# Kernel tuning notes

Hardware: AMD Instinct MI355X
Metric: run time of the kernel (lower is better)

The kernel has to match this reference:

```python
import jax, jax.numpy as jnp
import numpy as np

L, B, S, M, D, H, DK, FF = 4, 2, 512, 512, 1024, 16, 64, 4096


def setup_inputs() -> dict:
    key = jax.random.key(0)
    ks = jax.random.split(key, 16)
    std = 0.02
    inp = {
        'x': jax.random.normal(ks[0], (B, S, D), jnp.float32),
        'memory': jax.random.normal(ks[1], (L, B, M, D), jnp.float32),
        'Wq': jax.random.normal(ks[2], (L, D, D), jnp.float32) * std,
        'Wk': jax.random.normal(ks[3], (L, D, D), jnp.float32) * std,
        'Wv': jax.random.normal(ks[4], (L, D, D), jnp.float32) * std,
        'Wr': jax.random.normal(ks[5], (L, D, D), jnp.float32) * std,
        'Wo': jax.random.normal(ks[6], (L, D, D), jnp.float32) * std,
        'r_w_bias': jax.random.normal(ks[7], (L, H, DK), jnp.float32) * std,
        'r_r_bias': jax.random.normal(ks[8], (L, H, DK), jnp.float32) * std,
        'ln1_g': jnp.ones((L, D), jnp.float32),
        'ln1_b': jnp.zeros((L, D), jnp.float32),
        'ln2_g': jnp.ones((L, D), jnp.float32),
        'ln2_b': jnp.zeros((L, D), jnp.float32),
        'W1': jax.random.normal(ks[9], (L, D, FF), jnp.float32) * std,
        'b1': jnp.zeros((L, FF), jnp.float32),
        'W2': jax.random.normal(ks[10], (L, FF, D), jnp.float32) * std,
        'b2': jnp.zeros((L, D), jnp.float32),
    }
    return inp


def _pos_encodings(length, hidden):
    # sinusoidal encodings over [length-1 .. 0], sin/cos concat -> [length, hidden]
    pos = jnp.arange(length - 1, -1, -1, dtype=jnp.float32)
    freqs = jnp.arange(0, hidden, 2, dtype=jnp.float32)
    inv_freq = 1.0 / (10000.0 ** (freqs / hidden))
    ang = pos[:, None] * inv_freq[None, :]  # [T, D/2]
    return jnp.concatenate([jnp.sin(ang), jnp.cos(ang)], axis=-1)  # [T, D]


def _rel_shift(x):
    # x: [B, H, T1, T2] -> Transformer-XL relative shift
    b, h, t1, t2 = x.shape
    x = jnp.pad(x, ((0, 0), (0, 0), (0, 0), (1, 0)))
    x = x.reshape(b, h, t2 + 1, t1)[:, :, 1:]
    return x.reshape(b, h, t1, t2)


def _layernorm(x, g, b, eps=1e-5):
    mu = jnp.mean(x, axis=-1, keepdims=True)
    var = jnp.var(x, axis=-1, keepdims=True)
    return (x - mu) * jax.lax.rsqrt(var + eps) * g + b


def reference(x, memory, Wq, Wk, Wv, Wr, Wo, r_w_bias, r_r_bias,
              ln1_g, ln1_b, ln2_g, ln2_b, W1, b1, W2, b2):
    T = S + M
    pos = _pos_encodings(T, D)  # [T, D]
    # future mask with zero block for memory columns: [1,1,S,T]
    fut = jnp.triu(jnp.ones((S, S), jnp.float32), k=1) * (-1e6)
    mask = jnp.concatenate([jnp.zeros((S, M), jnp.float32), fut], axis=1)[None, None]
    scale = DK ** (-0.5)

    h = x
    for l in range(L):
        kv_in = jnp.concatenate([memory[l], h], axis=1)  # [B, T, D]
        q = jnp.einsum('bsd,dhk->bhsk', h, Wq[l].reshape(D, H, DK)) * scale
        k = jnp.einsum('btd,dhk->bhtk', kv_in, Wk[l].reshape(D, H, DK))
        v = jnp.einsum('btd,dhk->bhtk', kv_in, Wv[l].reshape(D, H, DK))
        r = jnp.einsum('td,dhk->htk', pos, Wr[l].reshape(D, H, DK))

        content = jnp.einsum('bhsk,bhtk->bhst', q + r_w_bias[l][None, :, None, :], k)
        rel = jnp.einsum('bhsk,htk->bhst', q + r_r_bias[l][None, :, None, :], r)
        logits = content + _rel_shift(rel) + mask  # [B,H,S,T]
        w = jax.nn.softmax(logits, axis=-1)
        attn = jnp.einsum('bhst,bhtk->bshk', w, v).reshape(B, S, D)
        attn = attn @ Wo[l]  # merge linear
        h = _layernorm(h + attn, ln1_g[l], ln1_b[l])

        ff = jax.nn.relu(h @ W1[l] + b1[l]) @ W2[l] + b2[l]
        h = _layernorm(h + ff, ln2_g[l], ln2_b[l])
    return h
```

## Files before the change

kernel.cpp:

```cpp
#include <hip/hip_runtime.h>
#include <math.h>

#define CB  2
#define CS  512
#define CM  512
#define CD  1024
#define CH  16
#define CDK 64
#define CFF 4096
#define CL  4
#define CT  1024

using short8 = __attribute__((ext_vector_type(8))) short;
using f32x4  = __attribute__((ext_vector_type(4))) float;

__device__ __forceinline__ ushort f2bf(float x) {
    union { float f; unsigned int u; } c; c.f = x;
    unsigned int u = c.u + 0x7FFFu + ((c.u >> 16) & 1u);
    return (ushort)(u >> 16);
}
__device__ __forceinline__ float bf2f(ushort h) {
    union { unsigned int u; float f; } c; c.u = ((unsigned int)h) << 16;
    return c.f;
}

#define GLD16(gsrc, ldst) \
    __builtin_amdgcn_global_load_lds((const __attribute__((address_space(1))) void*)(gsrc), \
                                     (__attribute__((address_space(3))) void*)(ldst), 16, 0, 0)

__global__ void pos_kernel(ushort* __restrict__ pos) {
    int idx = blockIdx.x * blockDim.x + threadIdx.x;
    if (idx >= CT * (CD / 2)) return;
    int i = idx % (CD / 2);
    int t = idx / (CD / 2);
    float p = (float)(CT - 1 - t);
    float inv = __expf(-(float)i * (9.210340371976184f / 512.0f));
    float ang = p * inv;
    pos[(size_t)t * CD + i]          = f2bf(sinf(ang));
    pos[(size_t)t * CD + i + CD / 2] = f2bf(cosf(ang));
}

__global__ void cvt_bf16_kernel(const float* __restrict__ in, ushort* __restrict__ out, int n8) {
    int i = blockIdx.x * blockDim.x + threadIdx.x;
    if (i >= n8) return;
    float4 a = ((const float4*)in)[i * 2];
    float4 c = ((const float4*)in)[i * 2 + 1];
    union { ushort us[8]; uint4 q; } pk;
    pk.us[0] = f2bf(a.x); pk.us[1] = f2bf(a.y); pk.us[2] = f2bf(a.z); pk.us[3] = f2bf(a.w);
    pk.us[4] = f2bf(c.x); pk.us[5] = f2bf(c.y); pk.us[6] = f2bf(c.z); pk.us[7] = f2bf(c.w);
    ((uint4*)out)[i] = pk.q;
}

__global__ __launch_bounds__(256)
void transpose_w5(const float* __restrict__ Wq, const float* __restrict__ Wk,
                  const float* __restrict__ Wv, const float* __restrict__ Wr,
                  const float* __restrict__ Wo,
                  ushort* __restrict__ wqkvT, ushort* __restrict__ wrT,
                  ushort* __restrict__ woT) {
    const size_t WD = (size_t)CD * CD;
    const int wi = blockIdx.z / CL, l = blockIdx.z % CL;
    const float* in;
    ushort* o;
    float sc = 1.0f;
    switch (wi) {
        case 0: in = Wq + l * WD; o = wqkvT + (size_t)l * 3 * WD; sc = 0.125f; break;
        case 1: in = Wk + l * WD; o = wqkvT + (size_t)l * 3 * WD + WD; break;
        case 2: in = Wv + l * WD; o = wqkvT + (size_t)l * 3 * WD + 2 * WD; break;
        case 3: in = Wr + l * WD; o = wrT + (size_t)l * WD; break;
        default: in = Wo + l * WD; o = woT + (size_t)l * WD; break;
    }
    __shared__ __align__(16) float t[64][68];
    const int n0 = blockIdx.x * 64, k0 = blockIdx.y * 64;
    const int tid = threadIdx.x;
    #pragma unroll
    for (int rep = 0; rep < 4; ++rep) {
        int lin = rep * 256 + tid;
        int r = lin >> 4, c4 = lin & 15;
        float4 v = *(const float4*)&in[(size_t)(k0 + r) * CD + n0 + c4 * 4];
        *(float4*)&t[r][c4 * 4] = v;
    }
    __syncthreads();
    #pragma unroll
    for (int rep = 0; rep < 2; ++rep) {
        int lin = rep * 256 + tid;
        int n = lin >> 3, kc = lin & 7;
        union { ushort us[8]; uint4 q; } pk;
        #pragma unroll
        for (int j = 0; j < 8; ++j) pk.us[j] = f2bf(t[kc * 8 + j][n] * sc);
        *(uint4*)&o[(size_t)(n0 + n) * CD + k0 + kc * 8] = pk.q;
    }
}

__global__ __launch_bounds__(256)
void transpose_cvt(const float* __restrict__ inb, ushort* __restrict__ outb,
                   int Kd, int Nc, size_t inz, size_t outz) {
    const float* in = inb + (size_t)blockIdx.z * inz;
    ushort* o = outb + (size_t)blockIdx.z * outz;
    __shared__ __align__(16) float t[64][68];
    const int n0 = blockIdx.x * 64, k0 = blockIdx.y * 64;
    const int tid = threadIdx.x;
    #pragma unroll
    for (int rep = 0; rep < 4; ++rep) {
        int lin = rep * 256 + tid;
        int r = lin >> 4, c4 = lin & 15;
        float4 v = *(const float4*)&in[(size_t)(k0 + r) * Nc + n0 + c4 * 4];
        *(float4*)&t[r][c4 * 4] = v;
    }
    __syncthreads();
    #pragma unroll
    for (int rep = 0; rep < 2; ++rep) {
        int lin = rep * 256 + tid;
        int n = lin >> 3, kc = lin & 7;
        union { ushort us[8]; uint4 q; } pk;
        #pragma unroll
        for (int j = 0; j < 8; ++j) pk.us[j] = f2bf(t[kc * 8 + j][n]);
        *(uint4*)&o[(size_t)(n0 + n) * Kd + k0 + kc * 8] = pk.q;
    }
}

template<int BM, int BN>
__global__ __launch_bounds__(256)
void gemm_bf16(const ushort* __restrict__ A, const ushort* __restrict__ Bt,
               float* __restrict__ Cf, ushort* __restrict__ Cbf,
               int Nc, int Kd, int lda, int cw, int ch,
               size_t az, size_t bz, size_t cz,
               const float* __restrict__ bias, float scale, int relu)
{
    constexpr int FM = BM / 32, FN = BN / 32;
    __shared__ __align__(16) ushort As[2][BM * 64];
    __shared__ __align__(16) ushort Bs[2][BN * 64];
    const int tid  = threadIdx.x;
    const int lane = tid & 63, w = tid >> 6;
    const int wr = w >> 1, wc = w & 1;
    const int lo4 = lane & 15, g = lane >> 4;
    const int id  = blockIdx.y * gridDim.x + blockIdx.x;
    const int e = id & 7, q = id >> 3;
    const int ncx = gridDim.x / cw;
    const int col0 = ((e % ncx) * cw + q % cw) * BN;
    const int row0 = ((e / ncx) * ch + q / cw) * BM;
    const int zz = blockIdx.z;
    const ushort* Ab = A  + (size_t)row0 * lda + (size_t)zz * az;
    const ushort* Bb = Bt + (size_t)col0 * lda + (size_t)zz * bz;
    f32x4 acc[FM][FN];
    #pragma unroll
    for (int m = 0; m < FM; ++m)
        #pragma unroll
        for (int n = 0; n < FN; ++n) acc[m][n] = (f32x4){0.f, 0.f, 0.f, 0.f};

#define GSTAGE(buf, kk) do {                                                          \
        _Pragma("unroll")                                                             \
        for (int c = 0; c < BM / 32; ++c) {                                           \
            const int linw = (c * 4 + w) * 64;                                        \
            const int lin  = linw + lane;                                             \
            GLD16(Ab + (size_t)(lin >> 3) * lda + (kk) + ((lin ^ (lin >> 3)) & 7) * 8, \
                  &As[buf][linw * 8]);                                                \
        }                                                                             \
        _Pragma("unroll")                                                             \
        for (int c = 0; c < BN / 32; ++c) {                                           \
            const int linw = (c * 4 + w) * 64;                                        \
            const int lin  = linw + lane;                                             \
            GLD16(Bb + (size_t)(lin >> 3) * lda + (kk) + ((lin ^ (lin >> 3)) & 7) * 8, \
                  &Bs[buf][linw * 8]);                                                \
        }                                                                             \
    } while (0)

    GSTAGE(0, 0);
    __syncthreads();
    int cur = 0;
    for (int k0 = 0; k0 < Kd; k0 += 64) {
        if (k0 + 64 < Kd) GSTAGE(cur ^ 1, k0 + 64);
        #pragma unroll
        for (int h2 = 0; h2 < 2; ++h2) {
            short8 af[FM], bfr[FN];
            #pragma unroll
            for (int m = 0; m < FM; ++m) {
                const int ar = wr * (BM / 2) + m * 16 + lo4;
                af[m] = *(const short8*)&As[cur][ar * 64 + ((((h2 << 2) + g) ^ (ar & 7)) << 3)];
            }
            #pragma unroll
            for (int n = 0; n < FN; ++n) {
                const int br = wc * (BN / 2) + n * 16 + lo4;
                bfr[n] = *(const short8*)&Bs[cur][br * 64 + ((((h2 << 2) + g) ^ (br & 7)) << 3)];
            }
            __builtin_amdgcn_s_setprio(1);
            #pragma unroll
            for (int m = 0; m < FM; ++m)
                #pragma unroll
                for (int n = 0; n < FN; ++n)
                    acc[m][n] = __builtin_amdgcn_mfma_f32_16x16x32_bf16(af[m], bfr[n], acc[m][n], 0, 0, 0);
            __builtin_amdgcn_s_setprio(0);
        }
        __syncthreads();
        cur ^= 1;
    }
#undef GSTAGE

    float*  Cw  = Cf  ? Cf  + (size_t)zz * cz : nullptr;
    ushort* Cbw = Cbf ? Cbf + (size_t)zz * cz : nullptr;
    const int colbase = col0 + wc * (BN / 2) + lo4;
    const int rowbase = row0 + wr * (BM / 2) + (g << 2);
    #pragma unroll
    for (int n = 0; n < FN; ++n) {
        const int col = colbase + n * 16;
        const float bv = bias ? bias[col] : 0.f;
        #pragma unroll
        for (int m = 0; m < FM; ++m) {
            #pragma unroll
            for (int r = 0; r < 4; ++r) {
                const int row = rowbase + m * 16 + r;
                float v = acc[m][n][r] * scale + bv;
                if (relu) v = fmaxf(v, 0.f);
                if (Cw)  Cw[(size_t)row * Nc + col] = v;
                if (Cbw) Cbw[(size_t)row * Nc + col] = f2bf(v);
            }
        }
    }
}

__global__ __launch_bounds__(256, 4)
void attn_kernel(const ushort* __restrict__ hproj, const ushort* __restrict__ kvmem,
                 const ushort* __restrict__ rbm,
                 const float* __restrict__ rwb, const float* __restrict__ rrb,
                 float* __restrict__ pw)
{
    const int id  = blockIdx.y * 32 + blockIdx.x;
    const int swz = (id & 7) * 64 + (id >> 3);
    const int zt = (swz & 31) >> 1, js = swz & 1;
    const int hh = swz >> 5, bb = blockIdx.z;
    const int q0 = zt * 32;
    __shared__ __align__(16) ushort Ks[64 * 64];
    __shared__ __align__(16) ushort Rs[96 * 64];
    __shared__ __align__(16) ushort Vt[80][72];
    __shared__ __align__(16) ushort Pl[4][16][40];
    __shared__ float mB[2][16], lB[2][16];
    const int tid = threadIdx.x;
    const int lane = tid & 63, w = tid >> 6;
    const int iw = w & 1, jh = w >> 1;
    const int g = lane >> 4, lo4 = lane & 15;

    for (int idx = tid; idx < 16 * 36; idx += 256)
        *(uint*)&Vt[64 + idx / 36][(idx % 36) * 2] = 0x3F803F80u;

    short8 aqw[2], aqr[2];
    {
        const ushort* qrow = hproj + ((size_t)(bb * CS + q0 + iw * 16 + lo4)) * 3072 + hh * CDK;
        const float* bw = rwb + hh * CDK;
        const float* br = rrb + hh * CDK;
        #pragma unroll
        for (int c = 0; c < 2; ++c) {
            const int kb = c * 32 + g * 8;
            uint4 qv = *(const uint4*)&qrow[kb];
            const ushort* qe = (const ushort*)&qv;
            #pragma unroll
            for (int e = 0; e < 8; ++e) {
                float qf = bf2f(qe[e]);
                aqw[c][e] = (short)f2bf(qf + bw[kb + e]);
                aqr[c][e] = (short)f2bf(qf + br[kb + e]);
            }
        }
    }

    const ushort* kvmB = kvmem + (size_t)bb * CM * 2048;
    const ushort* hpjB = hproj + (size_t)bb * CS * 3072;
    const ushort* rb2  = rbm + hh * CDK;
    const int jp = tid & 31, c8v = tid >> 5;

    float mr[4] = {-1e29f, -1e29f, -1e29f, -1e29f};
    f32x4 oacc[5];
    #pragma unroll
    for (int n = 0; n < 5; ++n) oacc[n] = (f32x4){0.f, 0.f, 0.f, 0.f};

    const int nt   = (q0 + 31 + CM) / 64 + 1;
    const int half = nt >> 1;
    const int t0 = js ? half : 0;
    const int t1 = js ? nt : half;

    for (int tt = t0; tt < t1; ++tt) {
        const int j0 = tt * 64;
        const int bnd = j0 + 480 - q0;
        const int isMem = (j0 < CM);
        const ushort* kb2 = isMem ? (kvmB + hh * CDK) : (hpjB + 1024 + hh * CDK);
        const ushort* vb2 = isMem ? (kvmB + 1024 + hh * CDK) : (hpjB + 2048 + hh * CDK);
        const int rstr = isMem ? 2048 : 3072;
        const int jloc = isMem ? j0 : (j0 - CM);
        __syncthreads();
        #pragma unroll
        for (int c = 0; c < 2; ++c) {
            const int linw = (c * 4 + w) * 64;
            const int lin  = linw + lane;
            const int row = lin >> 3, kc = lin & 7;
            GLD16(kb2 + (size_t)(jloc + row) * rstr + ((kc ^ (row & 7)) * 8),
                  Ks + linw * 8);
        }
        #pragma unroll
        for (int rep = 0; rep < 3; ++rep) {
            const int linw = (rep * 4 + w) * 64;
            const int lin  = linw + lane;
            const int row = lin >> 3, kc = lin & 7;
            int trel = bnd + row;
            trel = trel < 0 ? 0 : (trel > CT - 1 ? CT - 1 : trel);
            GLD16(rb2 + (size_t)trel * CD + ((kc ^ (row & 7)) * 8),
                  Rs + linw * 8);
        }
        {
            uint4 v0 = *(const uint4*)(vb2 + (size_t)(jloc + 2 * jp) * rstr + c8v * 8);
            uint4 v1 = *(const uint4*)(vb2 + (size_t)(jloc + 2 * jp + 1) * rstr + c8v * 8);
            const ushort* p0 = (const ushort*)&v0;
            const ushort* p1 = (const ushort*)&v1;
            #pragma unroll
            for (int e = 0; e < 8; ++e)
                *(uint*)&Vt[c8v * 8 + e][2 * jp] = (uint)p0[e] | ((uint)p1[e] << 16);
        }
        __syncthreads();

        f32x4 sa[2];
        sa[0] = (f32x4){0.f, 0.f, 0.f, 0.f};
        sa[1] = (f32x4){0.f, 0.f, 0.f, 0.f};
        f32x4 ra[3];
        #pragma unroll
        for (int mm = 0; mm < 3; ++mm) ra[mm] = (f32x4){0.f, 0.f, 0.f, 0.f};
        const int wb16 = jh * 32 - iw * 16 + 16;
        __builtin_amdgcn_s_setprio(1);
        #pragma unroll
        for (int c = 0; c < 2; ++c) {
            #pragma unroll
            for (int m16 = 0; m16 < 2; ++m16) {
                const int krow = jh * 32 + m16 * 16 + lo4;
                short8 bk = *(const short8*)&Ks[krow * 64 + ((((c << 2) + g) ^ (krow & 7)) << 3)];
                sa[m16] = __builtin_amdgcn_mfma_f32_16x16x32_bf16(aqw[c], bk, sa[m16], 0, 0, 0);
            }
            #pragma unroll
            for (int mm = 0; mm < 3; ++mm) {
                const int rrow = wb16 + mm * 16 + lo4;
                short8 brr = *(const short8*)&Rs[rrow * 64 + ((((c << 2) + g) ^ (rrow & 7)) << 3)];
                ra[mm] = __builtin_amdgcn_mfma_f32_16x16x32_bf16(aqr[c], brr, ra[mm], 0, 0, 0);
            }
        }
        __builtin_amdgcn_s_setprio(0);

        #pragma unroll
        for (int r = 0; r < 4; ++r) {
            const int il = 4 * g + r;
            const int dlo = lo4 + 15 - il;
            const int srcl = (lane & 48) | (dlo & 15);
            const int hi = dlo >> 4;
            float va = __shfl(ra[0][r], srcl);
            float vb = __shfl(ra[1][r], srcl);
            float vc = __shfl(ra[2][r], srcl);
            const float rel0 = hi ? vb : va;
            const float rel1 = hi ? vc : vb;
            const int ig = q0 + iw * 16 + il;
            const int jbase = j0 + jh * 32 + lo4;
            float s0 = (jbase      <= ig + CM) ? (sa[0][r] + rel0) : -1e30f;
            float s1 = (jbase + 16 <= ig + CM) ? (sa[1][r] + rel1) : -1e30f;
            float tm = fmaxf(s0, s1);
            #pragma unroll
            for (int off = 1; off < 16; off <<= 1) tm = fmaxf(tm, __shfl_xor(tm, off));
            const float mn = fmaxf(mr[r], tm);
            const float scl = __expf(mr[r] - mn);
            mr[r] = mn;
            Pl[w][il][lo4]      = f2bf(__expf(s0 - mn));
            Pl[w][il][16 + lo4] = f2bf(__expf(s1 - mn));
            #pragma unroll
            for (int n = 0; n < 5; ++n) oacc[n][r] *= scl;
        }

        __builtin_amdgcn_s_setprio(1);
        {
            short8 pa = *(const short8*)&Pl[w][lo4][g * 8];
            #pragma unroll
            for (int n = 0; n < 4; ++n) {
                short8 vb = *(const short8*)&Vt[n * 16 + lo4][jh * 32 + g * 8];
                oacc[n] = __builtin_amdgcn_mfma_f32_16x16x32_bf16(pa, vb, oacc[n], 0, 0, 0);
            }
            short8 vo = *(const short8*)&Vt[64 + lo4][jh * 32 + g * 8];
            oacc[4] = __builtin_amdgcn_mfma_f32_16x16x32_bf16(pa, vo, oacc[4], 0, 0, 0);
        }
        __builtin_amdgcn_s_setprio(0);
    }

    __syncthreads();
    float* oTmp = (float*)&Rs[0];
    if (jh == 1) {
        #pragma unroll
        for (int r = 0; r < 4; ++r) {
            const int il = 4 * g + r;
            #pragma unroll
            for (int n = 0; n < 4; ++n)
                oTmp[((iw * 16 + il) << 6) + n * 16 + lo4] = oacc[n][r];
            if (lo4 == 0) { mB[iw][il] = mr[r]; lB[iw][il] = oacc[4][r]; }
        }
    }
    __syncthreads();
    if (jh == 0) {
        float* pwp = pw + ((size_t)(((bb * CH + hh) * 16 + zt) * 2 + js)) * 2112;
        #pragma unroll
        for (int r = 0; r < 4; ++r) {
            const int il = 4 * g + r;
            const int row = iw * 16 + il;
            const float mBv = mB[iw][il], lBv = lB[iw][il];
            const float ms = fmaxf(mr[r], mBv);
            const float fA = __expf(mr[r] - ms);
            const float fB = __expf(mBv - ms);
            const float lt = oacc[4][r] * fA + lBv * fB;
            #pragma unroll
            for (int n = 0; n < 4; ++n)
                pwp[(row << 6) + n * 16 + lo4] =
                    oacc[n][r] * fA + oTmp[(row << 6) + n * 16 + lo4] * fB;
            if (lo4 == 0) { pwp[2048 + row] = ms; pwp[2048 + 32 + row] = lt; }
        }
    }
}

__global__ __launch_bounds__(256)
void attn_merge(const float* __restrict__ pw, ushort* __restrict__ outm) {
    const int zt = blockIdx.x, hh = blockIdx.y, bb = blockIdx.z;
    const int tid = threadIdx.x;
    const int row = tid >> 3, c8 = tid & 7;
    const float* pA = pw + ((size_t)(((bb * CH + hh) * 16 + zt) * 2 + 0)) * 2112;
    const float* pB = pA + 2112;
    const float mA = pA[2048 + row], lA = pA[2048 + 32 + row];
    const float mBv = pB[2048 + row], lBv = pB[2048 + 32 + row];
    const float ms = fmaxf(mA, mBv);
    const float fA = __expf(mA - ms);
    const float fB = __expf(mBv - ms);
    const float invl = 1.0f / (lA * fA + lBv * fB);
    float4 a0 = *(const float4*)&pA[(row << 6) + c8 * 8];
    float4 a1 = *(const float4*)&pA[(row << 6) + c8 * 8 + 4];
    float4 b0 = *(const float4*)&pB[(row << 6) + c8 * 8];
    float4 b1 = *(const float4*)&pB[(row << 6) + c8 * 8 + 4];
    union { ushort us[8]; uint4 q; } pk;
    pk.us[0] = f2bf((a0.x * fA + b0.x * fB) * invl);
    pk.us[1] = f2bf((a0.y * fA + b0.y * fB) * invl);
    pk.us[2] = f2bf((a0.z * fA + b0.z * fB) * invl);
    pk.us[3] = f2bf((a0.w * fA + b0.w * fB) * invl);
    pk.us[4] = f2bf((a1.x * fA + b1.x * fB) * invl);
    pk.us[5] = f2bf((a1.y * fA + b1.y * fB) * invl);
    pk.us[6] = f2bf((a1.z * fA + b1.z * fB) * invl);
    pk.us[7] = f2bf((a1.w * fA + b1.w * fB) * invl);
    *(uint4*)&outm[((size_t)(bb * CS + zt * 32 + row)) * CD + hh * CDK + c8 * 8] = pk.q;
}

__global__ __launch_bounds__(256)
void ln_kernel(const float* __restrict__ a, const float* __restrict__ p0,
               const float* __restrict__ p1, const float* __restrict__ bias,
               const float* __restrict__ g, const float* __restrict__ beta,
               float* __restrict__ out, ushort* __restrict__ outbf)
{
    const int row = blockIdx.x;
    const int tid = threadIdx.x;
    const size_t base = (size_t)row * CD;
    float4 xa = *(const float4*)&a[base + tid * 4];
    float4 x0v = *(const float4*)&p0[base + tid * 4];
    float4 x1v = *(const float4*)&p1[base + tid * 4];
    float4 bb = bias ? *(const float4*)&bias[tid * 4] : make_float4(0.f, 0.f, 0.f, 0.f);
    float x0 = xa.x + x0v.x + x1v.x + bb.x;
    float x1 = xa.y + x0v.y + x1v.y + bb.y;
    float x2 = xa.z + x0v.z + x1v.z + bb.z;
    float x3 = xa.w + x0v.w + x1v.w + bb.w;
    float sum = x0 + x1 + x2 + x3;
    float sq  = x0 * x0 + x1 * x1 + x2 * x2 + x3 * x3;
    #pragma unroll
    for (int off = 1; off < 64; off <<= 1) {
        sum += __shfl_xor(sum, off);
        sq  += __shfl_xor(sq, off);
    }
    __shared__ float ssum[4], ssq[4];
    const int wid = tid >> 6;
    if ((tid & 63) == 0) { ssum[wid] = sum; ssq[wid] = sq; }
    __syncthreads();
    sum = ssum[0] + ssum[1] + ssum[2] + ssum[3];
    sq  = ssq[0] + ssq[1] + ssq[2] + ssq[3];
    const float mean = sum * (1.0f / CD);
    const float var  = sq * (1.0f / CD) - mean * mean;
    const float rstd = rsqrtf(var + 1e-5f);
    float4 gv = *(const float4*)&g[tid * 4];
    float4 bv = *(const float4*)&beta[tid * 4];
    float4 r;
    r.x = (x0 - mean) * rstd * gv.x + bv.x;
    r.y = (x1 - mean) * rstd * gv.y + bv.y;
    r.z = (x2 - mean) * rstd * gv.z + bv.z;
    r.w = (x3 - mean) * rstd * gv.w + bv.w;
    *(float4*)&out[base + tid * 4] = r;
    if (outbf) {
        union { ushort us[4]; uint2 q; } pk;
        pk.us[0] = f2bf(r.x); pk.us[1] = f2bf(r.y); pk.us[2] = f2bf(r.z); pk.us[3] = f2bf(r.w);
        *(uint2*)&outbf[base + tid * 4] = pk.q;
    }
}

extern "C" void kernel_launch(void* const* d_in, const int* in_sizes, int n_in,
                              void* d_out, int out_size, void* d_ws, size_t ws_size,
                              hipStream_t stream) {
    const float* x    = (const float*)d_in[0];
    const float* memL = (const float*)d_in[1];
    const float* Wq   = (const float*)d_in[2];
    const float* Wk   = (const float*)d_in[3];
    const float* Wv   = (const float*)d_in[4];
    const float* Wr   = (const float*)d_in[5];
    const float* Wo   = (const float*)d_in[6];
    const float* rwb  = (const float*)d_in[7];
    const float* rrb  = (const float*)d_in[8];
    const float* ln1g = (const float*)d_in[9];
    const float* ln1b = (const float*)d_in[10];
    const float* ln2g = (const float*)d_in[11];
    const float* ln2b = (const float*)d_in[12];
    const float* W1   = (const float*)d_in[13];
    const float* b1   = (const float*)d_in[14];
    const float* W2   = (const float*)d_in[15];
    const float* b2   = (const float*)d_in[16];

    const size_t MEG = 1048576;
    float* h      = (float*)d_ws;
    float* p0     = h + MEG;
    float* p1     = p0 + MEG;
    float* pw     = p1 + MEG;
    ushort* hbf   = (ushort*)(pw + 1024 * 2112);
    ushort* membf = hbf + MEG;
    ushort* kvmem = membf + 4 * MEG;
    ushort* hproj = kvmem + 8 * MEG;
    ushort* attbf = hproj + 3 * MEG;
    ushort* ff1bf = attbf + MEG;
    ushort* posbf = ff1bf + 4 * MEG;
    ushort* r_all = posbf + MEG;
    ushort* wqkvT = r_all + 4 * MEG;
    ushort* wrT   = wqkvT + 12 * MEG;
    ushort* woT   = wrT + 4 * MEG;
    ushort* w1T   = woT + 4 * MEG;
    ushort* w2T   = w1T + 16 * MEG;

    const size_t WD = (size_t)CD * CD;

    pos_kernel<<<(CT * (CD / 2)) / 256, 256, 0, stream>>>(posbf);
    cvt_bf16_kernel<<<(CL * CB * CM * CD / 8) / 256, 256, 0, stream>>>(
        memL, membf, CL * CB * CM * CD / 8);
    cvt_bf16_kernel<<<(CB * CS * CD / 8) / 256, 256, 0, stream>>>(
        x, hbf, CB * CS * CD / 8);
    transpose_w5<<<dim3(16, 16, 5 * CL), 256, 0, stream>>>(Wq, Wk, Wv, Wr, Wo, wqkvT, wrT, woT);
    transpose_cvt<<<dim3(64, 16, CL), 256, 0, stream>>>(W1, w1T, CD, CFF, 4 * WD, 4 * WD);
    transpose_cvt<<<dim3(16, 64, CL), 256, 0, stream>>>(W2, w2T, CFF, CD, 4 * WD, 4 * WD);
    gemm_bf16<64, 64><<<dim3(16, 16, CL), 256, 0, stream>>>(
        posbf, wrT, nullptr, r_all, CD, CD, CD, 4, 8, 0, WD, (size_t)CT * CD,
        nullptr, 1.0f, 0);
    gemm_bf16<64, 128><<<dim3(16, 16, CL), 256, 0, stream>>>(
        membf, wqkvT + WD, nullptr, kvmem,
        2 * CD, CD, CD, 4, 8, MEG, 3 * WD, 2 * MEG, nullptr, 1.0f, 0);

    for (int l = 0; l < CL; ++l) {
        const float* hin = (l == 0) ? x : h;

        gemm_bf16<64, 128><<<dim3(24, 16), 256, 0, stream>>>(
            hbf, wqkvT + (size_t)l * 3 * WD, nullptr, hproj,
            3 * CD, CD, CD, 6, 8, 0, 0, 0, nullptr, 1.0f, 0);

        attn_kernel<<<dim3(2 * CS / 32, CH, CB), 256, 0, stream>>>(
            hproj, kvmem + (size_t)l * 2 * MEG, r_all + (size_t)l * CT * CD,
            rwb + (size_t)l * CH * CDK, rrb + (size_t)l * CH * CDK, pw);
        attn_merge<<<dim3(CS / 32, CH, CB), 256, 0, stream>>>(pw, attbf);

        gemm_bf16<64, 64><<<dim3(16, 16, 2), 256, 0, stream>>>(
            attbf, woT + (size_t)l * WD, p0, nullptr,
            CD, CD / 2, CD, 4, 8, CD / 2, CD / 2, MEG, nullptr, 1.0f, 0);
        ln_kernel<<<CB * CS, 256, 0, stream>>>(
            hin, p0, p1, nullptr, ln1g + (size_t)l * CD, ln1b + (size_t)l * CD, h, hbf);

        gemm_bf16<64, 128><<<dim3(32, 16), 256, 0, stream>>>(
            hbf, w1T + (size_t)l * 4 * WD, nullptr, ff1bf,
            CFF, CD, CD, 8, 8, 0, 0, 0, b1 + (size_t)l * CFF, 1.0f, 1);
        gemm_bf16<64, 64><<<dim3(16, 16, 2), 256, 0, stream>>>(
            ff1bf, w2T + (size_t)l * 4 * WD, p0, nullptr,
            CD, CFF / 2, CFF, 4, 8, CFF / 2, CFF / 2, MEG, nullptr, 1.0f, 0);
        ln_kernel<<<CB * CS, 256, 0, stream>>>(
            h, p0, p1, b2 + (size_t)l * CD, ln2g + (size_t)l * CD, ln2b + (size_t)l * CD,
            (l == CL - 1) ? (float*)d_out : h,
            (l == CL - 1) ? nullptr : hbf);
    }
}
```

Measured before the change: 597.6 us.

## Switch bf16 GEMM to a four-stage 32-wide K pipeline with explicit vmcnt waits

Replaces the double-buffered 64-wide K tile with a four-deep ring of 32-wide K tiles, using a new XOR swizzle for the narrower rows. Explicit s_waitcnt vmcnt and raw barriers let three future stages stay in flight while the current one is consumed. The goal is to hide global-to-LDS latency better. In exchange there are two barriers per step over half as much MFMA work, and the fixed vmcnt threshold does not shrink in the tail, where fewer loads are outstanding. That risks reading a stage before its load has finished.

```diff
diff --git a/kernel.cpp b/kernel.cpp
--- a/kernel.cpp
+++ b/kernel.cpp
@@ -127,8 +127,9 @@
                const float* __restrict__ bias, float scale, int relu)
 {
     constexpr int FM = BM / 32, FN = BN / 32;
-    __shared__ __align__(16) ushort As[2][BM * 64];
-    __shared__ __align__(16) ushort Bs[2][BN * 64];
+    constexpr int LPW = (BM + BN) / 64;
+    __shared__ __align__(16) ushort As[4][BM * 32];
+    __shared__ __align__(16) ushort Bs[4][BN * 32];
     const int tid  = threadIdx.x;
     const int lane = tid & 63, w = tid >> 6;
     const int wr = w >> 1, wc = w & 1;
@@ -149,49 +150,55 @@
 
 #define GSTAGE(buf, kk) do {                                                          \
         _Pragma("unroll")                                                             \
-        for (int c = 0; c < BM / 32; ++c) {                                           \
+        for (int c = 0; c < BM / 64; ++c) {                                           \
             const int linw = (c * 4 + w) * 64;                                        \
             const int lin  = linw + lane;                                             \
-            GLD16(Ab + (size_t)(lin >> 3) * lda + (kk) + ((lin ^ (lin >> 3)) & 7) * 8, \
+            const int row = lin >> 2, kc = lin & 3;                                   \
+            GLD16(Ab + (size_t)row * lda + (kk) + ((kc ^ ((row >> 1) & 3)) * 8),      \
                   &As[buf][linw * 8]);                                                \
         }                                                                             \
         _Pragma("unroll")                                                             \
-        for (int c = 0; c < BN / 32; ++c) {                                           \
+        for (int c = 0; c < BN / 64; ++c) {                                           \
             const int linw = (c * 4 + w) * 64;                                        \
             const int lin  = linw + lane;                                             \
-            GLD16(Bb + (size_t)(lin >> 3) * lda + (kk) + ((lin ^ (lin >> 3)) & 7) * 8, \
+            const int row = lin >> 2, kc = lin & 3;                                   \
+            GLD16(Bb + (size_t)row * lda + (kk) + ((kc ^ ((row >> 1) & 3)) * 8),      \
                   &Bs[buf][linw * 8]);                                                \
         }                                                                             \
     } while (0)
 
+    const int nsteps = Kd / 32;
     GSTAGE(0, 0);
-    __syncthreads();
-    int cur = 0;
-    for (int k0 = 0; k0 < Kd; k0 += 64) {
-        if (k0 + 64 < Kd) GSTAGE(cur ^ 1, k0 + 64);
-        #pragma unroll
-        for (int h2 = 0; h2 < 2; ++h2) {
-            short8 af[FM], bfr[FN];
-            #pragma unroll
-            for (int m = 0; m < FM; ++m) {
-                const int ar = wr * (BM / 2) + m * 16 + lo4;
-                af[m] = *(const short8*)&As[cur][ar * 64 + ((((h2 << 2) + g) ^ (ar & 7)) << 3)];
-            }
-            #pragma unroll
-            for (int n = 0; n < FN; ++n) {
-                const int br = wc * (BN / 2) + n * 16 + lo4;
-                bfr[n] = *(const short8*)&Bs[cur][br * 64 + ((((h2 << 2) + g) ^ (br & 7)) << 3)];
-            }
-            __builtin_amdgcn_s_setprio(1);
-            #pragma unroll
-            for (int m = 0; m < FM; ++m)
-                #pragma unroll
-                for (int n = 0; n < FN; ++n)
-                    acc[m][n] = __builtin_amdgcn_mfma_f32_16x16x32_bf16(af[m], bfr[n], acc[m][n], 0, 0, 0);
-            __builtin_amdgcn_s_setprio(0);
-        }
-        __syncthreads();
-        cur ^= 1;
+    GSTAGE(1, 32);
+    GSTAGE(2, 64);
+    GSTAGE(3, 96);
+    for (int s = 0; s < nsteps; ++s) {
+        const int buf = s & 3;
+        asm volatile("s_waitcnt vmcnt(%0)" :: "n"(3 * LPW) : "memory");
+        __builtin_amdgcn_s_barrier();
+        __builtin_amdgcn_sched_barrier(0);
+        short8 af[FM], bfr[FN];
+        #pragma unroll
+        for (int m = 0; m < FM; ++m) {
+            const int ar = wr * (BM / 2) + m * 16 + lo4;
+            af[m] = *(const short8*)&As[buf][ar * 32 + ((g ^ ((ar >> 1) & 3)) << 3)];
+        }
+        #pragma unroll
+        for (int n = 0; n < FN; ++n) {
+            const int br = wc * (BN / 2) + n * 16 + lo4;
+            bfr[n] = *(const short8*)&Bs[buf][br * 32 + ((g ^ ((br >> 1) & 3)) << 3)];
+        }
+        asm volatile("s_waitcnt lgkmcnt(0)" ::: "memory");
+        __builtin_amdgcn_sched_barrier(0);
+        __builtin_amdgcn_s_barrier();
+        if (s + 4 < nsteps) GSTAGE(buf, (s + 4) * 32);
+        __builtin_amdgcn_s_setprio(1);
+        #pragma unroll
+        for (int m = 0; m < FM; ++m)
+            #pragma unroll
+            for (int n = 0; n < FN; ++n)
+                acc[m][n] = __builtin_amdgcn_mfma_f32_16x16x32_bf16(af[m], bfr[n], acc[m][n], 0, 0, 0);
+        __builtin_amdgcn_s_setprio(0);
     }
 #undef GSTAGE
 
```

Measured after the change: 605.4 us. No clear change (+1.3%).
